# Performance work log

Measured on AMD Instinct MI355X. Metric: run time of the kernel, lower is better.

The kernel has to match this reference:

```python
import jax, jax.numpy as jnp
import numpy as np

HIDDEN = 256
NUM_STEPS = 3
N_NODES = 200000
N_GRAPHS = 512


def setup_inputs() -> dict:
    key = jax.random.key(0)
    ks = jax.random.split(key, 8)
    h = HIDDEN
    x = jax.random.normal(ks[0], (N_NODES, h), dtype=jnp.float32)
    batch = jnp.sort(jax.random.randint(ks[1], (N_NODES,), 0, N_GRAPHS)).astype(jnp.int64)
    s_ih = 1.0 / np.sqrt(2 * h)
    s_hh = 1.0 / np.sqrt(h)
    # LSTM (input 2h -> hidden h), PyTorch gate order i,f,g,o
    W_ih = jax.random.uniform(ks[2], (4 * h, 2 * h), jnp.float32, -s_ih, s_ih)
    W_hh = jax.random.uniform(ks[3], (4 * h, h), jnp.float32, -s_hh, s_hh)
    b_ih = jax.random.uniform(ks[4], (4 * h,), jnp.float32, -s_hh, s_hh)
    b_hh = jax.random.uniform(ks[5], (4 * h,), jnp.float32, -s_hh, s_hh)
    # out_proj: Linear(2h -> h)
    s_o = 1.0 / np.sqrt(2 * h)
    W_out = jax.random.uniform(ks[6], (h, 2 * h), jnp.float32, -s_o, s_o)
    b_out = jax.random.uniform(ks[7], (h,), jnp.float32, -s_o, s_o)
    return {"x": x, "batch": batch, "W_ih": W_ih, "W_hh": W_hh,
            "b_ih": b_ih, "b_hh": b_hh, "W_out": W_out, "b_out": b_out,
            "n_graphs": N_GRAPHS}


def _set2set(x, batch, W_ih, W_hh, b_ih, b_hh, n_graphs):
    h = x.shape[1]
    hs = jnp.zeros((n_graphs, h), x.dtype)
    cs = jnp.zeros((n_graphs, h), x.dtype)
    q_star = jnp.zeros((n_graphs, 2 * h), x.dtype)
    for _ in range(NUM_STEPS):
        # LSTM step (PyTorch gate order: i, f, g, o)
        gates = q_star @ W_ih.T + hs @ W_hh.T + (b_ih + b_hh)  # [B, 4h]
        i_g, f_g, g_g, o_g = jnp.split(gates, 4, axis=-1)
        cs = jax.nn.sigmoid(f_g) * cs + jax.nn.sigmoid(i_g) * jnp.tanh(g_g)
        hs = jax.nn.sigmoid(o_g) * jnp.tanh(cs)
        q = hs  # [B, h]
        # attention logits per node
        e = jnp.sum(x * q[batch], axis=-1)  # [N]
        # segment softmax over nodes of each graph
        m = jax.ops.segment_max(e, batch, num_segments=n_graphs)
        a = jnp.exp(e - m[batch])
        denom = jax.ops.segment_sum(a, batch, num_segments=n_graphs)
        a = a / denom[batch]
        # weighted readout
        r = jax.ops.segment_sum(a[:, None] * x, batch, num_segments=n_graphs)  # [B, h]
        q_star = jnp.concatenate([q, r], axis=-1)  # [B, 2h]
    return q_star


def reference(x, batch, W_ih, W_hh, b_ih, b_hh, W_out, b_out, n_graphs):
    q_star = _set2set(x, batch.astype(jnp.int32), W_ih, W_hh, b_ih, b_hh, n_graphs)
    return q_star @ W_out.T + b_out
```

## Files before the change

kernel.cpp:

```cpp
#include <hip/hip_runtime.h>
#include <hip/hip_bf16.h>

#define HID 256
#define NG 512

__device__ __forceinline__ float sigmoidf_(float v) { return 1.f / (1.f + __expf(-v)); }

__global__ __launch_bounds__(256) void prep_kernel(
    const float* __restrict__ W_ih, const float* __restrict__ W_hh,
    const float* __restrict__ b_ih, const float* __restrict__ b_hh,
    const int* __restrict__ batch, int n,
    float* __restrict__ Wcat, float* __restrict__ bcat, int* __restrict__ starts)
{
    int b = blockIdx.x, tid = threadIdx.x;
    if (b < 512) {
        int o = (b * 256 + tid) * 4;
        int k = o & 511, row = o >> 9;
        float4 v = *(const float4*)&W_ih[o];
        if (k < 256) {
            float4 u = *(const float4*)&W_hh[row * 256 + k];
            v.x += u.x; v.y += u.y; v.z += u.z; v.w += u.w;
        }
        *(float4*)&Wcat[o] = v;
    } else if (b < 516) {
        int i = (b - 512) * 256 + tid;
        bcat[i] = b_ih[i] + b_hh[i];
    } else {
        int g = (b - 516) * 256 + tid;
        if (g > NG) return;
        if (g == NG) { starts[NG] = n; return; }
        int lo = 0, hi = n;
        while (lo < hi) {
            int mid = (lo + hi) >> 1;
            if (batch[mid] < g) lo = mid + 1; else hi = mid;
        }
        starts[g] = lo;
    }
}

__global__ __launch_bounds__(256, 2) void attn_kernel(
    const float* __restrict__ x, const int* __restrict__ starts,
    const float* __restrict__ gp, const float* __restrict__ bcat,
    float* __restrict__ cs, float* __restrict__ qs, int step0)
{
    __shared__ __align__(16) float ql[HID];
    __shared__ __align__(16) float red[4][HID];
    __shared__ float mw[4], lw[4];

    const int g = blockIdx.x;
    const int tid = threadIdx.x;

    float ig, fg, gg, og;
    if (step0) {
        ig = bcat[tid]; fg = bcat[256 + tid]; gg = bcat[512 + tid]; og = bcat[768 + tid];
    } else {
        const float* a0 = gp + (size_t)g * 1024;
        const float* a1 = a0 + (size_t)512 * 1024;
        ig = a0[tid]       + a1[tid]       + bcat[tid];
        fg = a0[256 + tid] + a1[256 + tid] + bcat[256 + tid];
        gg = a0[512 + tid] + a1[512 + tid] + bcat[512 + tid];
        og = a0[768 + tid] + a1[768 + tid] + bcat[768 + tid];
    }
    float cp = step0 ? 0.f : cs[g * HID + tid];
    float cn = sigmoidf_(fg) * cp + sigmoidf_(ig) * tanhf(gg);
    float h  = sigmoidf_(og) * tanhf(cn);
    cs[g * HID + tid] = cn;
    qs[(size_t)g * 512 + tid] = h;
    ql[tid] = h;

    const int s0 = starts[g];
    const int nn = starts[g + 1] - s0;
    if (nn <= 0) { qs[(size_t)g * 512 + HID + tid] = 0.f; return; }
    __syncthreads();

    const int w = tid >> 6, lane = tid & 63;
    const int j = lane >> 3;
    const int s = lane & 7;

    float4 qf[8];
    #pragma unroll
    for (int k = 0; k < 8; ++k) qf[k] = *(const float4*)&ql[k * 32 + s * 4];

    const int nch = (nn + 7) >> 3;
    const int last = s0 + nn - 1;
    const float NEG = -3.402823466e38f;

    float m_run = NEG, l_run = 0.f;
    float4 racc[8] = {};
    float4 xA[8], xB[8];

    if (w < nch) {
        int node = s0 + w * 8 + j; if (node > last) node = last;
        const float* bp = x + (size_t)node * HID + s * 4;
        #pragma unroll
        for (int k = 0; k < 8; ++k) xA[k] = *(const float4*)(bp + k * 32);
    }
    if (w + 4 < nch) {
        int node = s0 + (w + 4) * 8 + j; if (node > last) node = last;
        const float* bp = x + (size_t)node * HID + s * 4;
        #pragma unroll
        for (int k = 0; k < 8; ++k) xB[k] = *(const float4*)(bp + k * 32);
    }

    #define PROCESS(XB, CC)                                                   \
    {                                                                         \
        const bool valid = ((CC) * 8 + j) < nn;                               \
        float e = 0.f;                                                        \
        _Pragma("unroll")                                                     \
        for (int k = 0; k < 8; ++k)                                           \
            e += XB[k].x * qf[k].x + XB[k].y * qf[k].y                        \
               + XB[k].z * qf[k].z + XB[k].w * qf[k].w;                       \
        e += __shfl_xor(e, 1); e += __shfl_xor(e, 2); e += __shfl_xor(e, 4);  \
        e = valid ? e : NEG;                                                  \
        float m_new = fmaxf(m_run, e);                                        \
        float alpha = __expf(m_run - m_new);                                  \
        float p = valid ? __expf(e - m_new) : 0.f;                            \
        l_run = l_run * alpha + p;                                            \
        m_run = m_new;                                                        \
        _Pragma("unroll")                                                     \
        for (int k = 0; k < 8; ++k) {                                         \
            racc[k].x = racc[k].x * alpha + p * XB[k].x;                      \
            racc[k].y = racc[k].y * alpha + p * XB[k].y;                      \
            racc[k].z = racc[k].z * alpha + p * XB[k].z;                      \
            racc[k].w = racc[k].w * alpha + p * XB[k].w;                      \
        }                                                                     \
    }

    int c = w;
    for (; c + 4 < nch; c += 8) {
        {
            float4 xn[8];
            if (c + 8 < nch) {
                int node = s0 + (c + 8) * 8 + j; if (node > last) node = last;
                const float* bp = x + (size_t)node * HID + s * 4;
                #pragma unroll
                for (int k = 0; k < 8; ++k) xn[k] = *(const float4*)(bp + k * 32);
            }
            PROCESS(xA, c);
            #pragma unroll
            for (int k = 0; k < 8; ++k) xA[k] = xn[k];
        }
        {
            float4 xn[8];
            if (c + 12 < nch) {
                int node = s0 + (c + 12) * 8 + j; if (node > last) node = last;
                const float* bp = x + (size_t)node * HID + s * 4;
                #pragma unroll
                for (int k = 0; k < 8; ++k) xn[k] = *(const float4*)(bp + k * 32);
            }
            PROCESS(xB, c + 4);
            #pragma unroll
            for (int k = 0; k < 8; ++k) xB[k] = xn[k];
        }
    }
    if (c < nch) PROCESS(xA, c);
    #undef PROCESS

    #pragma unroll
    for (int bit = 8; bit <= 32; bit <<= 1) {
        float m2 = __shfl_xor(m_run, bit);
        float l2 = __shfl_xor(l_run, bit);
        float M  = fmaxf(m_run, m2);
        float a1 = __expf(m_run - M), a2 = __expf(m2 - M);
        l_run = l_run * a1 + l2 * a2;
        #pragma unroll
        for (int k = 0; k < 8; ++k) {
            racc[k].x = racc[k].x * a1 + __shfl_xor(racc[k].x, bit) * a2;
            racc[k].y = racc[k].y * a1 + __shfl_xor(racc[k].y, bit) * a2;
            racc[k].z = racc[k].z * a1 + __shfl_xor(racc[k].z, bit) * a2;
            racc[k].w = racc[k].w * a1 + __shfl_xor(racc[k].w, bit) * a2;
        }
        m_run = M;
    }
    if (j == 0) {
        #pragma unroll
        for (int k = 0; k < 8; ++k) *(float4*)&red[w][k * 32 + s * 4] = racc[k];
        if (s == 0) { mw[w] = m_run; lw[w] = l_run; }
    }
    __syncthreads();

    float M = fmaxf(fmaxf(mw[0], mw[1]), fmaxf(mw[2], mw[3]));
    float f0 = __expf(mw[0] - M), f1 = __expf(mw[1] - M);
    float f2 = __expf(mw[2] - M), f3 = __expf(mw[3] - M);
    float L = lw[0] * f0 + lw[1] * f1 + lw[2] * f2 + lw[3] * f3;
    float r = red[0][tid] * f0 + red[1][tid] * f1 + red[2][tid] * f2 + red[3][tid] * f3;
    qs[(size_t)g * 512 + HID + tid] = r / L;
}

__global__ __launch_bounds__(256) void gemm_splitk(
    const float* __restrict__ A, int lda,
    const float* __restrict__ B, int ldb,
    float* __restrict__ Cp, int ldc, int KS, size_t slice_stride)
{
    __shared__ float As[16][76];
    __shared__ float Bs[16][76];
    const int tid = threadIdx.x;
    const int tx = tid & 15, ty = tid >> 4;
    const int m0 = blockIdx.y * 64, n0 = blockIdx.x * 64;
    const int kb = blockIdx.z * KS;
    const int r = tid >> 2, kc = (tid & 3) << 2;
    float acc[4][4] = {};

    const float* Ap = &A[(size_t)(m0 + r) * lda + kb + kc];
    const float* Bp = &B[(size_t)(n0 + r) * ldb + kb + kc];
    float4 av = *(const float4*)Ap;
    float4 bv = *(const float4*)Bp;

    for (int k0 = 0; k0 < KS; k0 += 16) {
        As[kc + 0][r] = av.x; As[kc + 1][r] = av.y; As[kc + 2][r] = av.z; As[kc + 3][r] = av.w;
        Bs[kc + 0][r] = bv.x; Bs[kc + 1][r] = bv.y; Bs[kc + 2][r] = bv.z; Bs[kc + 3][r] = bv.w;
        __syncthreads();
        if (k0 + 16 < KS) {
            av = *(const float4*)(Ap + k0 + 16);
            bv = *(const float4*)(Bp + k0 + 16);
        }
        #pragma unroll
        for (int kk = 0; kk < 16; ++kk) {
            float4 a = *(const float4*)&As[kk][ty << 2];
            float4 b = *(const float4*)&Bs[kk][tx << 2];
            acc[0][0] += a.x * b.x; acc[0][1] += a.x * b.y; acc[0][2] += a.x * b.z; acc[0][3] += a.x * b.w;
            acc[1][0] += a.y * b.x; acc[1][1] += a.y * b.y; acc[1][2] += a.y * b.z; acc[1][3] += a.y * b.w;
            acc[2][0] += a.z * b.x; acc[2][1] += a.z * b.y; acc[2][2] += a.z * b.z; acc[2][3] += a.z * b.w;
            acc[3][0] += a.w * b.x; acc[3][1] += a.w * b.y; acc[3][2] += a.w * b.z; acc[3][3] += a.w * b.w;
        }
        __syncthreads();
    }
    float* out = Cp + blockIdx.z * slice_stride;
    #pragma unroll
    for (int i = 0; i < 4; ++i) {
        float4 o = make_float4(acc[i][0], acc[i][1], acc[i][2], acc[i][3]);
        *(float4*)&out[(size_t)(m0 + ty * 4 + i) * ldc + n0 + (tx << 2)] = o;
    }
}

__global__ __launch_bounds__(256) void finalize_out(
    const float* __restrict__ op, const float* __restrict__ b_out,
    float* __restrict__ out)
{
    int i = blockIdx.x * 256 + threadIdx.x;
    if (i < 512 * 256) {
        out[i] = op[i] + op[131072 + i] + op[262144 + i] + op[393216 + i] + b_out[i & 255];
    }
}

extern "C" void kernel_launch(void* const* d_in, const int* in_sizes, int n_in,
                              void* d_out, int out_size, void* d_ws, size_t ws_size,
                              hipStream_t stream)
{
    const float* x     = (const float*)d_in[0];
    const int*   batch = (const int*)d_in[1];
    const float* W_ih  = (const float*)d_in[2];
    const float* W_hh  = (const float*)d_in[3];
    const float* b_ih  = (const float*)d_in[4];
    const float* b_hh  = (const float*)d_in[5];
    const float* W_out = (const float*)d_in[6];
    const float* b_out = (const float*)d_in[7];
    float* out = (float*)d_out;
    const int n = in_sizes[1];
    (void)n_in; (void)out_size; (void)ws_size;

    char* ws = (char*)d_ws;
    float* qs     = (float*)(ws);
    float* cs     = (float*)(ws + 0x100000);
    float* gp     = (float*)(ws + 0x180000);
    float* Wcat   = (float*)(ws + 0x580000);
    float* bcat   = (float*)(ws + 0x780000);
    int*   starts = (int*)  (ws + 0x781000);
    float* op     = (float*)(ws + 0x790000);

    prep_kernel<<<519, 256, 0, stream>>>(W_ih, W_hh, b_ih, b_hh, batch, n,
                                         Wcat, bcat, starts);
    for (int step = 0; step < 3; ++step) {
        if (step > 0) {
            gemm_splitk<<<dim3(16, 8, 2), 256, 0, stream>>>(
                qs, 512, Wcat, 512, gp, 1024, 256, (size_t)512 * 1024);
        }
        attn_kernel<<<NG, 256, 0, stream>>>(x, starts, gp, bcat, cs, qs, step == 0);
    }
    gemm_splitk<<<dim3(4, 8, 4), 256, 0, stream>>>(
        qs, 512, W_out, 512, op, 256, 128, (size_t)512 * 256);
    finalize_out<<<512, 256, 0, stream>>>(op, b_out, out);
}
```

Baseline: 455.1 us.

## Restructure attention so each wavefront lane owns a float4 slice of every row

The attention kernel now gives each 64-lane wavefront four whole rows at a time, with each lane holding one float4 of the 256-wide row. Before, eight rows were spread across 8-lane groups, each lane holding eight float4s. This shrinks register use (racc drops from 8 float4 to 1), so the occupancy hint in launch_bounds is removed, and the cross-group merge at the end is gone. The cost is a full 6-step wave-wide shuffle reduction for every dot product and a serial loop with only one row group prefetched ahead. That leaves less memory-level parallelism per wave unless higher occupancy makes up for it.

```diff
diff --git a/kernel.cpp b/kernel.cpp
--- a/kernel.cpp
+++ b/kernel.cpp
@@ -38,7 +38,7 @@
     }
 }
 
-__global__ __launch_bounds__(256, 2) void attn_kernel(
+__global__ __launch_bounds__(256) void attn_kernel(
     const float* __restrict__ x, const int* __restrict__ starts,
     const float* __restrict__ gp, const float* __restrict__ bcat,
     float* __restrict__ cs, float* __restrict__ qs, int step0)
@@ -74,116 +74,87 @@
     __syncthreads();
 
     const int w = tid >> 6, lane = tid & 63;
-    const int j = lane >> 3;
-    const int s = lane & 7;
-
-    float4 qf[8];
-    #pragma unroll
-    for (int k = 0; k < 8; ++k) qf[k] = *(const float4*)&ql[k * 32 + s * 4];
-
-    const int nch = (nn + 7) >> 3;
-    const int last = s0 + nn - 1;
+    const float4 qv = *(const float4*)&ql[lane * 4];
+    const float* xg = x + (size_t)s0 * HID + lane * 4;
+    const int lastrow = nn - 1;
     const float NEG = -3.402823466e38f;
 
     float m_run = NEG, l_run = 0.f;
-    float4 racc[8] = {};
-    float4 xA[8], xB[8];
-
-    if (w < nch) {
-        int node = s0 + w * 8 + j; if (node > last) node = last;
-        const float* bp = x + (size_t)node * HID + s * 4;
+    float4 racc = make_float4(0.f, 0.f, 0.f, 0.f);
+    float4 y0, y1, y2, y3, z0, z1, z2, z3;
+
+    int row0 = 4 * w;
+    if (row0 < nn) {
+        int r1 = row0 + 1 > lastrow ? lastrow : row0 + 1;
+        int r2 = row0 + 2 > lastrow ? lastrow : row0 + 2;
+        int r3 = row0 + 3 > lastrow ? lastrow : row0 + 3;
+        y0 = *(const float4*)(xg + (size_t)row0 * HID);
+        y1 = *(const float4*)(xg + (size_t)r1 * HID);
+        y2 = *(const float4*)(xg + (size_t)r2 * HID);
+        y3 = *(const float4*)(xg + (size_t)r3 * HID);
+    }
+    for (; row0 < nn; row0 += 16) {
+        const int nr = row0 + 16;
+        if (nr < nn) {
+            int r1 = nr + 1 > lastrow ? lastrow : nr + 1;
+            int r2 = nr + 2 > lastrow ? lastrow : nr + 2;
+            int r3 = nr + 3 > lastrow ? lastrow : nr + 3;
+            z0 = *(const float4*)(xg + (size_t)nr * HID);
+            z1 = *(const float4*)(xg + (size_t)r1 * HID);
+            z2 = *(const float4*)(xg + (size_t)r2 * HID);
+            z3 = *(const float4*)(xg + (size_t)r3 * HID);
+        }
+        float d0 = y0.x * qv.x + y0.y * qv.y + y0.z * qv.z + y0.w * qv.w;
+        float d1 = y1.x * qv.x + y1.y * qv.y + y1.z * qv.z + y1.w * qv.w;
+        float d2 = y2.x * qv.x + y2.y * qv.y + y2.z * qv.z + y2.w * qv.w;
+        float d3 = y3.x * qv.x + y3.y * qv.y + y3.z * qv.z + y3.w * qv.w;
         #pragma unroll
-        for (int k = 0; k < 8; ++k) xA[k] = *(const float4*)(bp + k * 32);
-    }
-    if (w + 4 < nch) {
-        int node = s0 + (w + 4) * 8 + j; if (node > last) node = last;
-        const float* bp = x + (size_t)node * HID + s * 4;
-        #pragma unroll
-        for (int k = 0; k < 8; ++k) xB[k] = *(const float4*)(bp + k * 32);
-    }
-
-    #define PROCESS(XB, CC)                                                   \
-    {                                                                         \
-        const bool valid = ((CC) * 8 + j) < nn;                               \
-        float e = 0.f;                                                        \
-        _Pragma("unroll")                                                     \
-        for (int k = 0; k < 8; ++k)                                           \
-            e += XB[k].x * qf[k].x + XB[k].y * qf[k].y                        \
-               + XB[k].z * qf[k].z + XB[k].w * qf[k].w;                       \
-        e += __shfl_xor(e, 1); e += __shfl_xor(e, 2); e += __shfl_xor(e, 4);  \
-        e = valid ? e : NEG;                                                  \
-        float m_new = fmaxf(m_run, e);                                        \
-        float alpha = __expf(m_run - m_new);                                  \
-        float p = valid ? __expf(e - m_new) : 0.f;                            \
-        l_run = l_run * alpha + p;                                            \
-        m_run = m_new;                                                        \
-        _Pragma("unroll")                                                     \
-        for (int k = 0; k < 8; ++k) {                                         \
-            racc[k].x = racc[k].x * alpha + p * XB[k].x;                      \
-            racc[k].y = racc[k].y * alpha + p * XB[k].y;                      \
-            racc[k].z = racc[k].z * alpha + p * XB[k].z;                      \
-            racc[k].w = racc[k].w * alpha + p * XB[k].w;                      \
-        }                                                                     \
-    }
-
-    int c = w;
-    for (; c + 4 < nch; c += 8) {
-        {
-            float4 xn[8];
-            if (c + 8 < nch) {
-                int node = s0 + (c + 8) * 8 + j; if (node > last) node = last;
-                const float* bp = x + (size_t)node * HID + s * 4;
-                #pragma unroll
-                for (int k = 0; k < 8; ++k) xn[k] = *(const float4*)(bp + k * 32);
-            }
-            PROCESS(xA, c);
-            #pragma unroll
-            for (int k = 0; k < 8; ++k) xA[k] = xn[k];
-        }
-        {
-            float4 xn[8];
-            if (c + 12 < nch) {
-                int node = s0 + (c + 12) * 8 + j; if (node > last) node = last;
-                const float* bp = x + (size_t)node * HID + s * 4;
-                #pragma unroll
-                for (int k = 0; k < 8; ++k) xn[k] = *(const float4*)(bp + k * 32);
-            }
-            PROCESS(xB, c + 4);
-            #pragma unroll
-            for (int k = 0; k < 8; ++k) xB[k] = xn[k];
-        }
-    }
-    if (c < nch) PROCESS(xA, c);
-    #undef PROCESS
-
-    #pragma unroll
-    for (int bit = 8; bit <= 32; bit <<= 1) {
-        float m2 = __shfl_xor(m_run, bit);
-        float l2 = __shfl_xor(l_run, bit);
-        float M  = fmaxf(m_run, m2);
-        float a1 = __expf(m_run - M), a2 = __expf(m2 - M);
-        l_run = l_run * a1 + l2 * a2;
-        #pragma unroll
-        for (int k = 0; k < 8; ++k) {
-            racc[k].x = racc[k].x * a1 + __shfl_xor(racc[k].x, bit) * a2;
-            racc[k].y = racc[k].y * a1 + __shfl_xor(racc[k].y, bit) * a2;
-            racc[k].z = racc[k].z * a1 + __shfl_xor(racc[k].z, bit) * a2;
-            racc[k].w = racc[k].w * a1 + __shfl_xor(racc[k].w, bit) * a2;
-        }
-        m_run = M;
-    }
-    if (j == 0) {
-        #pragma unroll
-        for (int k = 0; k < 8; ++k) *(float4*)&red[w][k * 32 + s * 4] = racc[k];
-        if (s == 0) { mw[w] = m_run; lw[w] = l_run; }
-    }
+        for (int off = 1; off < 64; off <<= 1) {
+            d0 += __shfl_xor(d0, off);
+            d1 += __shfl_xor(d1, off);
+            d2 += __shfl_xor(d2, off);
+            d3 += __shfl_xor(d3, off);
+        }
+        const float e0 = d0;
+        const float e1 = (row0 + 1 < nn) ? d1 : NEG;
+        const float e2 = (row0 + 2 < nn) ? d2 : NEG;
+        const float e3 = (row0 + 3 < nn) ? d3 : NEG;
+        const float em = fmaxf(fmaxf(e0, e1), fmaxf(e2, e3));
+        if (em > m_run) {
+            const float alpha = __expf(m_run - em);
+            const float p0 = __expf(e0 - em);
+            const float p1 = __expf(e1 - em);
+            const float p2 = __expf(e2 - em);
+            const float p3 = __expf(e3 - em);
+            l_run = l_run * alpha + (p0 + p1) + (p2 + p3);
+            racc.x = racc.x * alpha + p0 * y0.x + p1 * y1.x + p2 * y2.x + p3 * y3.x;
+            racc.y = racc.y * alpha + p0 * y0.y + p1 * y1.y + p2 * y2.y + p3 * y3.y;
+            racc.z = racc.z * alpha + p0 * y0.z + p1 * y1.z + p2 * y2.z + p3 * y3.z;
+            racc.w = racc.w * alpha + p0 * y0.w + p1 * y1.w + p2 * y2.w + p3 * y3.w;
+            m_run = em;
+        } else {
+            const float p0 = __expf(e0 - m_run);
+            const float p1 = __expf(e1 - m_run);
+            const float p2 = __expf(e2 - m_run);
+            const float p3 = __expf(e3 - m_run);
+            l_run += (p0 + p1) + (p2 + p3);
+            racc.x += p0 * y0.x + p1 * y1.x + p2 * y2.x + p3 * y3.x;
+            racc.y += p0 * y0.y + p1 * y1.y + p2 * y2.y + p3 * y3.y;
+            racc.z += p0 * y0.z + p1 * y1.z + p2 * y2.z + p3 * y3.z;
+            racc.w += p0 * y0.w + p1 * y1.w + p2 * y2.w + p3 * y3.w;
+        }
+        y0 = z0; y1 = z1; y2 = z2; y3 = z3;
+    }
+
+    *(float4*)&red[w][lane * 4] = racc;
+    if (lane == 0) { mw[w] = m_run; lw[w] = l_run; }
     __syncthreads();
-
-    float M = fmaxf(fmaxf(mw[0], mw[1]), fmaxf(mw[2], mw[3]));
-    float f0 = __expf(mw[0] - M), f1 = __expf(mw[1] - M);
-    float f2 = __expf(mw[2] - M), f3 = __expf(mw[3] - M);
-    float L = lw[0] * f0 + lw[1] * f1 + lw[2] * f2 + lw[3] * f3;
-    float r = red[0][tid] * f0 + red[1][tid] * f1 + red[2][tid] * f2 + red[3][tid] * f3;
+    const float M = fmaxf(fmaxf(mw[0], mw[1]), fmaxf(mw[2], mw[3]));
+    const float f0 = __expf(mw[0] - M), f1 = __expf(mw[1] - M);
+    const float f2 = __expf(mw[2] - M), f3 = __expf(mw[3] - M);
+    const float L = lw[0] * f0 + lw[1] * f1 + lw[2] * f2 + lw[3] * f3;
+    const float r = red[0][tid] * f0 + red[1][tid] * f1
+                  + red[2][tid] * f2 + red[3][tid] * f3;
     qs[(size_t)g * 512 + HID + tid] = r / L;
 }
 
```

After: 413.5 us. -9.1%, faster.
